# Optimization experiments

Hardware: AMD Instinct MI355X
Metric: run time of the kernel (lower is better)

The kernel has to match this reference:

```python
import jax, jax.numpy as jnp
import numpy as np

N_WIN = 7      # region grid (BiFormer default)
NUM_HEADS = 8
TOPK = 4
EPS = 1e-5

def layernorm(x, g, b):
    mu = x.mean(-1, keepdims=True)
    var = ((x - mu) ** 2).mean(-1, keepdims=True)
    return (x - mu) * jax.lax.rsqrt(var + EPS) * g + b

def bilevel_routing_attn(x, wqkv, bqkv, wo, bo):
    B, H, W, C = x.shape
    h, w = H // N_WIN, W // N_WIN          # region size (8,8)
    R, r = N_WIN * N_WIN, h * w            # 49 regions, 64 tokens each
    d = C // NUM_HEADS
    scale = 1.0 / jnp.sqrt(jnp.asarray(d, x.dtype))
    qkv = x @ wqkv + bqkv                  # (B,H,W,3C)
    q, k, v = jnp.split(qkv, 3, axis=-1)
    def to_regions(t):
        t = t.reshape(B, N_WIN, h, N_WIN, w, C).transpose(0, 1, 3, 2, 4, 5)
        return t.reshape(B, R, r, C)
    qr, kr, vr = to_regions(q), to_regions(k), to_regions(v)
    # coarse region-level routing
    q_reg = qr.mean(2)                     # (B,R,C)
    k_reg = kr.mean(2)
    logits = jnp.einsum('brc,bsc->brs', q_reg, k_reg)   # (B,R,R)
    _, idx = jax.lax.top_k(logits, TOPK)   # (B,R,TOPK)
    # gather top-k regions' k/v: out[b,i,j] = kr[b, idx[b,i,j]]
    idx_e = idx[:, :, :, None, None]       # (B,R,TOPK,1,1)
    kg = jnp.take_along_axis(kr[:, None], idx_e, axis=2).reshape(B, R, TOPK * r, C)
    vg = jnp.take_along_axis(vr[:, None], idx_e, axis=2).reshape(B, R, TOPK * r, C)
    # fine-grained multi-head attention within routed regions
    qh = qr.reshape(B, R, r, NUM_HEADS, d)
    kh = kg.reshape(B, R, TOPK * r, NUM_HEADS, d)
    vh = vg.reshape(B, R, TOPK * r, NUM_HEADS, d)
    scores = jnp.einsum('brqhd,brkhd->brhqk', qh, kh) * scale
    attn = jax.nn.softmax(scores, axis=-1)
    out = jnp.einsum('brhqk,brkhd->brqhd', attn, vh).reshape(B, R, r, C)
    # regions back to image layout
    out = out.reshape(B, N_WIN, N_WIN, h, w, C).transpose(0, 1, 3, 2, 4, 5)
    out = out.reshape(B, H, W, C)
    return out @ wo + bo

def mlp(x, w1, bm1, w2, bm2):
    return jax.nn.gelu(x @ w1 + bm1) @ w2 + bm2

def setup_inputs() -> dict:
    key = jax.random.key(0)
    ks = jax.random.split(key, 5)
    C = 256
    s = lambda fan: 1.0 / np.sqrt(fan)
    return {
        'x': jax.random.normal(ks[0], (8, 56, 56, C), jnp.float32),
        'ln1_g': jnp.ones((C,), jnp.float32),
        'ln1_b': jnp.zeros((C,), jnp.float32),
        'wqkv': jax.random.normal(ks[1], (C, 3 * C), jnp.float32) * s(C),
        'bqkv': jnp.zeros((3 * C,), jnp.float32),
        'wo': jax.random.normal(ks[2], (C, C), jnp.float32) * s(C),
        'bo': jnp.zeros((C,), jnp.float32),
        'ln2_g': jnp.ones((C,), jnp.float32),
        'ln2_b': jnp.zeros((C,), jnp.float32),
        'w1': jax.random.normal(ks[3], (C, 4 * C), jnp.float32) * s(C),
        'bm1': jnp.zeros((4 * C,), jnp.float32),
        'w2': jax.random.normal(ks[4], (4 * C, C), jnp.float32) * s(4 * C),
        'bm2': jnp.zeros((C,), jnp.float32),
    }

def reference(x, ln1_g, ln1_b, wqkv, bqkv, wo, bo, ln2_g, ln2_b, w1, bm1, w2, bm2):
    x = x + bilevel_routing_attn(layernorm(x, ln1_g, ln1_b), wqkv, bqkv, wo, bo)
    x = x + mlp(layernorm(x, ln2_g, ln2_b), w1, bm1, w2, bm2)
    return x
```

## Files before the change

### kernel.cpp

```cpp
#include <hip/hip_runtime.h>
#include <math.h>

#define CDIM 256
#define QKVDIM 768
#define NHEADS 8
#define DHEAD 32
#define NWIN 7
#define NREG 49
#define TK 4
static constexpr int NROWS = 8 * 56 * 56;

typedef __attribute__((ext_vector_type(8))) short s16x8;
typedef __attribute__((ext_vector_type(4))) float f32x4;
typedef __attribute__((ext_vector_type(16))) float f32x16;
typedef unsigned short ushort_t;

union U4 { unsigned u[4]; s16x8 v; };

__device__ __forceinline__ ushort_t bfr(float f) {
    unsigned u = __float_as_uint(f);
    unsigned r = (u + 0x7FFFu + ((u >> 16) & 1u)) >> 16;
    return (ushort_t)r;
}
__device__ __forceinline__ float gelu_f(float x) {
    float u = 0.7978845608028654f * (x + 0.044715f * x * x * x);
    return 0.5f * x * (1.0f + tanhf(u));
}
__device__ __forceinline__ void glds16(const void* g, void* l) {
    __builtin_amdgcn_global_load_lds((const __attribute__((address_space(1))) void*)g,
                                     (__attribute__((address_space(3))) void*)l, 16, 0, 0);
}
template <int N>
__device__ __forceinline__ void waitvm() {
    if constexpr (N == 0) asm volatile("s_waitcnt vmcnt(0)" ::: "memory");
    else if constexpr (N == 3) asm volatile("s_waitcnt vmcnt(3)" ::: "memory");
    else if constexpr (N == 4) asm volatile("s_waitcnt vmcnt(4)" ::: "memory");
}
__device__ __forceinline__ void barrier_raw() {
    asm volatile("s_barrier" ::: "memory");
}
__device__ __forceinline__ f32x16 zero16() {
    f32x16 z;
#pragma unroll
    for (int i = 0; i < 16; i++) z[i] = 0.f;
    return z;
}

__global__ __launch_bounds__(256) void ln_kernel(const float* __restrict__ x,
                                                 const float* __restrict__ g,
                                                 const float* __restrict__ bparam,
                                                 ushort_t* __restrict__ y) {
    int wave = threadIdx.x >> 6, lane = threadIdx.x & 63;
    int row = blockIdx.x * 4 + wave;
    const float4* xr = (const float4*)(x + (size_t)row * CDIM);
    float4 v = xr[lane];
    float s = v.x + v.y + v.z + v.w;
    float s2 = v.x * v.x + v.y * v.y + v.z * v.z + v.w * v.w;
#pragma unroll
    for (int off = 32; off; off >>= 1) {
        s += __shfl_xor(s, off, 64);
        s2 += __shfl_xor(s2, off, 64);
    }
    float mu = s * (1.0f / CDIM);
    float rstd = rsqrtf(s2 * (1.0f / CDIM) - mu * mu + 1e-5f);
    float4 gv = ((const float4*)g)[lane];
    float4 bv = ((const float4*)bparam)[lane];
    ushort4 o;
    o.x = bfr((v.x - mu) * rstd * gv.x + bv.x);
    o.y = bfr((v.y - mu) * rstd * gv.y + bv.y);
    o.z = bfr((v.z - mu) * rstd * gv.z + bv.z);
    o.w = bfr((v.w - mu) * rstd * gv.w + bv.w);
    *(ushort4*)(y + (size_t)row * CDIM + lane * 4) = o;
}

__global__ __launch_bounds__(256) void ymean_kernel(const float* __restrict__ x,
                                                    const float* __restrict__ g,
                                                    const float* __restrict__ bparam,
                                                    float* __restrict__ ymean) {
    int blk = blockIdx.x;
    int b = blk / NREG, rid = blk % NREG;
    int ai = rid / NWIN, aj = rid % NWIN;
    int w = threadIdx.x >> 6, lane = threadIdx.x & 63;
    float4 gv = ((const float4*)g)[lane];
    float4 bv = ((const float4*)bparam)[lane];
    float4 acc = {0.f, 0.f, 0.f, 0.f};
    for (int it = 0; it < 16; it++) {
        int t = it * 4 + w;
        size_t row = ((size_t)(b * 56 + ai * 8 + (t >> 3))) * 56 + aj * 8 + (t & 7);
        float4 v = ((const float4*)(x + row * CDIM))[lane];
        float s = v.x + v.y + v.z + v.w;
        float s2 = v.x * v.x + v.y * v.y + v.z * v.z + v.w * v.w;
#pragma unroll
        for (int off = 32; off; off >>= 1) {
            s += __shfl_xor(s, off, 64);
            s2 += __shfl_xor(s2, off, 64);
        }
        float mu = s * (1.0f / CDIM);
        float rstd = rsqrtf(s2 * (1.0f / CDIM) - mu * mu + 1e-5f);
        acc.x += (v.x - mu) * rstd * gv.x + bv.x;
        acc.y += (v.y - mu) * rstd * gv.y + bv.y;
        acc.z += (v.z - mu) * rstd * gv.z + bv.z;
        acc.w += (v.w - mu) * rstd * gv.w + bv.w;
    }
    __shared__ float red[4][CDIM];
    *(float4*)&red[w][lane * 4] = acc;
    __syncthreads();
    if (w == 0) {
        float4 r0 = *(float4*)&red[0][lane * 4];
        float4 r1 = *(float4*)&red[1][lane * 4];
        float4 r2 = *(float4*)&red[2][lane * 4];
        float4 r3 = *(float4*)&red[3][lane * 4];
        float4 o;
        o.x = (r0.x + r1.x + r2.x + r3.x) * (1.0f / 64.0f);
        o.y = (r0.y + r1.y + r2.y + r3.y) * (1.0f / 64.0f);
        o.z = (r0.z + r1.z + r2.z + r3.z) * (1.0f / 64.0f);
        o.w = (r0.w + r1.w + r2.w + r3.w) * (1.0f / 64.0f);
        *(float4*)(ymean + (size_t)blk * CDIM + lane * 4) = o;
    }
}

__global__ __launch_bounds__(256) void regproj_kernel(const float* __restrict__ ymean,
                                                      const float* __restrict__ wqkv,
                                                      const float* __restrict__ bqkv,
                                                      float* __restrict__ qreg,
                                                      float* __restrict__ kreg) {
    int blk = blockIdx.x;
    __shared__ float ym[CDIM];
    ym[threadIdx.x] = ymean[(size_t)blk * CDIM + threadIdx.x];
    __syncthreads();
    int c = threadIdx.x;
    float sq = 0.f, sk = 0.f;
    for (int k = 0; k < CDIM; k++) {
        float yv = ym[k];
        sq = fmaf(yv, wqkv[(size_t)k * QKVDIM + c], sq);
        sk = fmaf(yv, wqkv[(size_t)k * QKVDIM + CDIM + c], sk);
    }
    qreg[(size_t)blk * CDIM + c] = sq + bqkv[c];
    kreg[(size_t)blk * CDIM + c] = sk + bqkv[CDIM + c];
}

__global__ __launch_bounds__(256) void wtrans_kernel(const float* __restrict__ src,
                                                     ushort_t* __restrict__ dst,
                                                     int K, int N) {
    __shared__ float t[32][33];
    int tx = threadIdx.x & 31, ty = threadIdx.x >> 5;
    int n0 = blockIdx.x * 32, k0 = blockIdx.y * 32;
#pragma unroll
    for (int i = 0; i < 4; i++) t[ty + i * 8][tx] = src[(size_t)(k0 + ty + i * 8) * N + n0 + tx];
    __syncthreads();
#pragma unroll
    for (int i = 0; i < 4; i++)
        dst[(size_t)(n0 + ty + i * 8) * K + k0 + tx] = bfr(t[tx][ty + i * 8]);
}

__global__ __launch_bounds__(256) void vtrans_kernel(const ushort_t* __restrict__ qkvbf,
                                                     ushort_t* __restrict__ vt) {
    __shared__ ushort_t t[32][34];
    int tx = threadIdx.x & 31, ty = threadIdx.x >> 5;
    int t0 = blockIdx.x * 32, c0 = blockIdx.y * 32, b = blockIdx.z;
#pragma unroll
    for (int i = 0; i < 4; i++)
        t[ty + i * 8][tx] = qkvbf[((size_t)b * 3136 + t0 + ty + i * 8) * QKVDIM + 512 + c0 + tx];
    __syncthreads();
#pragma unroll
    for (int i = 0; i < 4; i++)
        vt[((size_t)b * CDIM + c0 + ty + i * 8) * 3136 + t0 + tx] = t[tx][ty + i * 8];
}

template <int BM, int BN, int MODE>
__global__ __launch_bounds__(256) void mgemm(const ushort_t* __restrict__ A,
                                             const ushort_t* __restrict__ WT,
                                             const float* __restrict__ bias,
                                             const float* __restrict__ res,
                                             float* __restrict__ outf,
                                             ushort_t* __restrict__ outb,
                                             int N, int K) {
    constexpr int WM = BM / 2, WN = BN / 2, MI = WM / 16, NI = WN / 16;
    constexpr int RA = BM / 64, RB = BN / 64, L = RA + RB;
    __shared__ __align__(16) ushort_t As[2 * BM * 32];
    __shared__ __align__(16) ushort_t Bs[2 * BN * 32];
    const int tid = threadIdx.x, lane = tid & 63, w = tid >> 6;
    const int wm = w >> 1, wn = w & 1;

    const int gx = gridDim.x;
    const int nwg = gx * gridDim.y;
    const int bid = blockIdx.y * gx + blockIdx.x;
    const int lbid = (bid & 7) * (nwg >> 3) + (bid >> 3);
    const int tm = (lbid / gx) * BM, tn = (lbid % gx) * BN;

    f32x4 acc[MI][NI];
#pragma unroll
    for (int i = 0; i < MI; i++)
#pragma unroll
        for (int j = 0; j < NI; j++) acc[i][j] = (f32x4){0.f, 0.f, 0.f, 0.f};

    auto stage = [&](int buf, int k0) {
#pragma unroll
        for (int p = 0; p < RA; p++) {
            int row = (p * 4 + w) * 16 + (lane >> 2);
            int slot = lane & 3;
            int mr = (row ^ (row >> 2)) & 3;
            glds16(A + (size_t)(tm + row) * K + k0 + ((slot ^ mr) * 8),
                   (char*)As + buf * BM * 64 + (p * 4 + w) * 1024);
        }
#pragma unroll
        for (int p = 0; p < RB; p++) {
            int row = (p * 4 + w) * 16 + (lane >> 2);
            int slot = lane & 3;
            int mr = (row ^ (row >> 2)) & 3;
            glds16(WT + (size_t)(tn + row) * K + k0 + ((slot ^ mr) * 8),
                   (char*)Bs + buf * BN * 64 + (p * 4 + w) * 1024);
        }
    };

    const int NT = K >> 5;
    const int fr = lane & 15, sl = lane >> 4;
    stage(0, 0);
    for (int kt = 0; kt < NT; ++kt) {
        int cur = kt & 1;
        if (kt + 1 < NT) {
            stage(cur ^ 1, (kt + 1) * 32);
            waitvm<L>();
        } else {
            waitvm<0>();
        }
        barrier_raw();
        s16x8 af[MI], bfv[NI];
#pragma unroll
        for (int i = 0; i < MI; i++) {
            int rowa = wm * WM + i * 16 + fr;
            int ma = (rowa ^ (rowa >> 2)) & 3;
            af[i] = *(const s16x8*)&As[cur * BM * 32 + rowa * 32 + ((sl ^ ma) * 8)];
        }
#pragma unroll
        for (int j = 0; j < NI; j++) {
            int rowb = wn * WN + j * 16 + fr;
            int mb = (rowb ^ (rowb >> 2)) & 3;
            bfv[j] = *(const s16x8*)&Bs[cur * BN * 32 + rowb * 32 + ((sl ^ mb) * 8)];
        }
#pragma unroll
        for (int i = 0; i < MI; i++)
#pragma unroll
            for (int j = 0; j < NI; j++)
                acc[i][j] = __builtin_amdgcn_mfma_f32_16x16x32_bf16(af[i], bfv[j], acc[i][j], 0, 0, 0);
        barrier_raw();
    }

    const int cl = lane & 15, gq = lane >> 4;
#pragma unroll
    for (int j = 0; j < NI; j++) {
        int col = tn + wn * WN + j * 16 + cl;
        float bb = bias[col];
#pragma unroll
        for (int i = 0; i < MI; i++) {
            int rowb = tm + wm * WM + i * 16 + gq * 4;
#pragma unroll
            for (int r = 0; r < 4; r++) {
                float v = acc[i][j][r] + bb;
                size_t off = (size_t)(rowb + r) * N + col;
                if (MODE == 0) {
                    outb[off] = bfr(col < 256 ? v * 0.17677669529663687f : v);
                } else if (MODE == 1 || MODE == 3) {
                    outf[off] = v + res[off];
                } else {
                    outb[off] = bfr(gelu_f(v));
                }
            }
        }
    }
}

__global__ __launch_bounds__(64) void routing_kernel(const float* __restrict__ qreg,
                                                     const float* __restrict__ kreg,
                                                     int* __restrict__ idx) {
    int b = blockIdx.x / NREG;
    int row = blockIdx.x % NREG;
    int lane = threadIdx.x;
    float myv = -INFINITY;
    if (lane < NREG) {
        const float* qv = qreg + ((size_t)b * NREG + row) * CDIM;
        const float* kv = kreg + ((size_t)b * NREG + lane) * CDIM;
        float s = 0.f;
        for (int c = 0; c < CDIM; c++) s += qv[c] * kv[c];
        myv = s;
    }
    for (int t = 0; t < TK; t++) {
        float v = myv;
        int ix = lane;
#pragma unroll
        for (int off = 32; off; off >>= 1) {
            float ov = __shfl_xor(v, off, 64);
            int oi = __shfl_xor(ix, off, 64);
            if (ov > v || (ov == v && oi < ix)) { v = ov; ix = oi; }
        }
        if (lane == 0) idx[((size_t)b * NREG + row) * TK + t] = ix;
        if (lane == ix) myv = -INFINITY;
    }
}

__global__ __launch_bounds__(256) void attn2_kernel(const ushort_t* __restrict__ qk,
                                                    const ushort_t* __restrict__ vt,
                                                    const int* __restrict__ idx,
                                                    ushort_t* __restrict__ outb) {
    int wid = blockIdx.x * 4 + (threadIdx.x >> 6);
    int lane = threadIdx.x & 63;
    int g = lane >> 5, col = lane & 31;
    int qh = wid & 1;
    int h = (wid >> 1) & 7;
    int rr = wid >> 4;
    int rid = rr % NREG, b = rr / NREG;
    int ai = rid / NWIN, aj = rid % NWIN;

    int qtok = qh * 32 + col;
    size_t qrow_g = ((size_t)(b * 56 + ai * 8 + (qtok >> 3))) * 56 + aj * 8 + (qtok & 7);
    const s16x8 bq0 = *(const s16x8*)(qk + qrow_g * QKVDIM + h * 32 + g * 8);
    const s16x8 bq1 = *(const s16x8*)(qk + qrow_g * QKVDIM + h * 32 + 16 + g * 8);

    const int* ip = idx + (size_t)rr * TK;
    int regs[4] = {ip[0], ip[1], ip[2], ip[3]};

    float m_run = -1e30f, l_run = 0.f;
    f32x16 o = zero16();
    const size_t vtrowbase = ((size_t)(b * CDIM + h * 32 + col)) * 3136;

#pragma unroll
    for (int rc = 0; rc < 4; rc++) {
        int reg = regs[rc];
        int rai = reg / NWIN, raj = reg % NWIN;
        s16x8 ka[2][2];
#pragma unroll
        for (int mf = 0; mf < 2; mf++) {
            int ktok = mf * 32 + col;
            size_t krow_g = ((size_t)(b * 56 + rai * 8 + (ktok >> 3))) * 56 + raj * 8 + (ktok & 7);
#pragma unroll
            for (int kd = 0; kd < 2; kd++)
                ka[mf][kd] = *(const s16x8*)(qk + krow_g * QKVDIM + 256 + h * 32 + kd * 16 + g * 8);
        }
        f32x16 s0 = zero16(), s1 = zero16();
        s0 = __builtin_amdgcn_mfma_f32_32x32x16_bf16(ka[0][0], bq0, s0, 0, 0, 0);
        s0 = __builtin_amdgcn_mfma_f32_32x32x16_bf16(ka[0][1], bq1, s0, 0, 0, 0);
        s1 = __builtin_amdgcn_mfma_f32_32x32x16_bf16(ka[1][0], bq0, s1, 0, 0, 0);
        s1 = __builtin_amdgcn_mfma_f32_32x32x16_bf16(ka[1][1], bq1, s1, 0, 0, 0);

        float tmax = -1e30f;
#pragma unroll
        for (int i = 0; i < 16; i++) tmax = fmaxf(tmax, fmaxf(s0[i], s1[i]));
        tmax = fmaxf(tmax, __shfl_xor(tmax, 32, 64));

        float m_new = fmaxf(m_run, tmax);
        float f = __expf(m_run - m_new);
        l_run *= f;
#pragma unroll
        for (int r = 0; r < 16; r++) {
            int orow = (r & 3) + 8 * (r >> 2) + 4 * g;
            float fr = __shfl(f, orow, 64);
            o[r] *= fr;
        }
        m_run = m_new;

        float tsum = 0.f;
#pragma unroll
        for (int i = 0; i < 16; i++) {
            s0[i] = __expf(s0[i] - m_run);
            s1[i] = __expf(s1[i] - m_run);
            tsum += s0[i] + s1[i];
        }
        l_run += tsum + __shfl_xor(tsum, 32, 64);

#define PVSTEP(SS, CC, KS)                                                              \
    {                                                                                   \
        unsigned wa = (unsigned)bfr(SS[CC * 8 + 0]) | ((unsigned)bfr(SS[CC * 8 + 1]) << 16); \
        unsigned wb_ = (unsigned)bfr(SS[CC * 8 + 2]) | ((unsigned)bfr(SS[CC * 8 + 3]) << 16); \
        unsigned wc = (unsigned)bfr(SS[CC * 8 + 4]) | ((unsigned)bfr(SS[CC * 8 + 5]) << 16); \
        unsigned wd = (unsigned)bfr(SS[CC * 8 + 6]) | ((unsigned)bfr(SS[CC * 8 + 7]) << 16); \
        unsigned sxa = (unsigned)__shfl_xor((int)wa, 32, 64);                           \
        unsigned sxb = (unsigned)__shfl_xor((int)wb_, 32, 64);                          \
        unsigned sxc = (unsigned)__shfl_xor((int)wc, 32, 64);                           \
        unsigned sxd = (unsigned)__shfl_xor((int)wd, 32, 64);                           \
        U4 pw;                                                                          \
        pw.u[0] = g ? sxc : wa;                                                         \
        pw.u[1] = g ? sxd : wb_;                                                        \
        pw.u[2] = g ? wc : sxa;                                                         \
        pw.u[3] = g ? wd : sxb;                                                         \
        const s16x8 vb = *(const s16x8*)(vt + vtrowbase + (size_t)(rai * 8 + KS * 2 + g) * 56 + raj * 8); \
        o = __builtin_amdgcn_mfma_f32_32x32x16_bf16(pw.v, vb, o, 0, 0, 0);              \
    }
        PVSTEP(s0, 0, 0)
        PVSTEP(s0, 1, 1)
        PVSTEP(s1, 0, 2)
        PVSTEP(s1, 1, 3)
#undef PVSTEP
    }

#pragma unroll
    for (int r = 0; r < 16; r++) {
        int orow = (r & 3) + 8 * (r >> 2) + 4 * g;
        float lr = __shfl(l_run, orow, 64);
        float val = o[r] / lr;
        int tok = qh * 32 + orow;
        size_t row_g = ((size_t)(b * 56 + ai * 8 + (tok >> 3))) * 56 + aj * 8 + (tok & 7);
        outb[row_g * 256 + h * 32 + col] = bfr(val);
    }
}

extern "C" void kernel_launch(void* const* d_in, const int* in_sizes, int n_in,
                              void* d_out, int out_size, void* d_ws, size_t ws_size,
                              hipStream_t stream) {
    const float* x    = (const float*)d_in[0];
    const float* ln1g = (const float*)d_in[1];
    const float* ln1b = (const float*)d_in[2];
    const float* wqkv = (const float*)d_in[3];
    const float* bqkv = (const float*)d_in[4];
    const float* wo   = (const float*)d_in[5];
    const float* bo   = (const float*)d_in[6];
    const float* ln2g = (const float*)d_in[7];
    const float* ln2b = (const float*)d_in[8];
    const float* w1   = (const float*)d_in[9];
    const float* bm1  = (const float*)d_in[10];
    const float* w2   = (const float*)d_in[11];
    const float* bm2  = (const float*)d_in[12];
    float* out = (float*)d_out;
    char* ws = (char*)d_ws;

    ushort_t* ws_qkvbf = (ushort_t*)(ws);
    ushort_t* ws_hbf   = (ushort_t*)(ws + 38535168);
    ushort_t* ws_ybf   = (ushort_t*)(ws + 89915392);
    ushort_t* ws_vt    = (ushort_t*)(ws + 102760448);
    ushort_t* ws_attn  = (ushort_t*)(ws + 115605504);
    float*    ws_ymean = (float*)(ws + 128450560);
    float*    ws_qreg  = (float*)(ws + 128851968);
    float*    ws_kreg  = (float*)(ws + 129253376);
    int*      ws_idx   = (int*)(ws + 129654784);
    ushort_t* ws_wqkvT = (ushort_t*)(ws + 129661056);
    ushort_t* ws_woT   = (ushort_t*)(ws + 130054272);
    ushort_t* ws_w1T   = (ushort_t*)(ws + 130185344);
    ushort_t* ws_w2T   = (ushort_t*)(ws + 130709632);

    const int M = NROWS;

    wtrans_kernel<<<dim3(768 / 32, 256 / 32), 256, 0, stream>>>(wqkv, ws_wqkvT, 256, 768);
    wtrans_kernel<<<dim3(256 / 32, 256 / 32), 256, 0, stream>>>(wo, ws_woT, 256, 256);
    wtrans_kernel<<<dim3(1024 / 32, 256 / 32), 256, 0, stream>>>(w1, ws_w1T, 256, 1024);
    wtrans_kernel<<<dim3(256 / 32, 1024 / 32), 256, 0, stream>>>(w2, ws_w2T, 1024, 256);
    ln_kernel<<<M / 4, 256, 0, stream>>>(x, ln1g, ln1b, ws_ybf);
    ymean_kernel<<<8 * NREG, 256, 0, stream>>>(x, ln1g, ln1b, ws_ymean);
    regproj_kernel<<<8 * NREG, 256, 0, stream>>>(ws_ymean, wqkv, bqkv, ws_qreg, ws_kreg);
    routing_kernel<<<8 * NREG, 64, 0, stream>>>(ws_qreg, ws_kreg, ws_idx);
    mgemm<128, 128, 0><<<dim3(QKVDIM / 128, M / 128), 256, 0, stream>>>(
        ws_ybf, ws_wqkvT, bqkv, nullptr, nullptr, ws_qkvbf, QKVDIM, CDIM);
    vtrans_kernel<<<dim3(3136 / 32, 256 / 32, 8), 256, 0, stream>>>(ws_qkvbf, ws_vt);
    attn2_kernel<<<8 * NREG * NHEADS * 2 / 4, 256, 0, stream>>>(ws_qkvbf, ws_vt, ws_idx, ws_attn);
    mgemm<128, 64, 1><<<dim3(CDIM / 64, M / 128), 256, 0, stream>>>(
        ws_attn, ws_woT, bo, x, out, nullptr, CDIM, CDIM);
    ln_kernel<<<M / 4, 256, 0, stream>>>(out, ln2g, ln2b, ws_ybf);
    mgemm<128, 128, 2><<<dim3(1024 / 128, M / 128), 256, 0, stream>>>(
        ws_ybf, ws_w1T, bm1, nullptr, nullptr, ws_hbf, 1024, CDIM);
    mgemm<128, 64, 3><<<dim3(CDIM / 64, M / 128), 256, 0, stream>>>(
        ws_hbf, ws_w2T, bm2, out, out, nullptr, CDIM, 1024);
}
```

Before: 321.4 us.

## Stage bf16 GEMM epilogue through shared memory for vectorized stores, cheaper GELU

For the QKV and MLP-up GEMM modes, the epilogue now writes bf16 results into a padded shared-memory tile, reusing the A/B staging buffer. It then emits 16-byte row-contiguous global stores, replacing scattered 2-byte writes. The swizzle pattern for the LDS tiles changes to (row>>1)&3, and GELU's tanhf is replaced by an exp-based fast formula. The epilogue adds two block barriers and LDS traffic, and the fast exp GELU may differ slightly numerically.

```diff
diff --git a/kernel.cpp b/kernel.cpp
--- a/kernel.cpp
+++ b/kernel.cpp
@@ -24,7 +24,9 @@
 }
 __device__ __forceinline__ float gelu_f(float x) {
     float u = 0.7978845608028654f * (x + 0.044715f * x * x * x);
-    return 0.5f * x * (1.0f + tanhf(u));
+    float e = __expf(2.0f * u);
+    float t = 1.0f - __fdividef(2.0f, e + 1.0f);
+    return 0.5f * x * (1.0f + t);
 }
 __device__ __forceinline__ void glds16(const void* g, void* l) {
     __builtin_amdgcn_global_load_lds((const __attribute__((address_space(1))) void*)g,
@@ -177,8 +179,10 @@
                                              int N, int K) {
     constexpr int WM = BM / 2, WN = BN / 2, MI = WM / 16, NI = WN / 16;
     constexpr int RA = BM / 64, RB = BN / 64, L = RA + RB;
-    __shared__ __align__(16) ushort_t As[2 * BM * 32];
-    __shared__ __align__(16) ushort_t Bs[2 * BN * 32];
+    __shared__ __align__(16) char smem[2 * (BM + BN) * 64];
+    ushort_t* As = (ushort_t*)smem;
+    ushort_t* Bs = (ushort_t*)(smem + 2 * BM * 64);
+    ushort_t* Cs = (ushort_t*)smem;
     const int tid = threadIdx.x, lane = tid & 63, w = tid >> 6;
     const int wm = w >> 1, wn = w & 1;
 
@@ -199,7 +203,7 @@
         for (int p = 0; p < RA; p++) {
             int row = (p * 4 + w) * 16 + (lane >> 2);
             int slot = lane & 3;
-            int mr = (row ^ (row >> 2)) & 3;
+            int mr = (row >> 1) & 3;
             glds16(A + (size_t)(tm + row) * K + k0 + ((slot ^ mr) * 8),
                    (char*)As + buf * BM * 64 + (p * 4 + w) * 1024);
         }
@@ -207,7 +211,7 @@
         for (int p = 0; p < RB; p++) {
             int row = (p * 4 + w) * 16 + (lane >> 2);
             int slot = lane & 3;
-            int mr = (row ^ (row >> 2)) & 3;
+            int mr = (row >> 1) & 3;
             glds16(WT + (size_t)(tn + row) * K + k0 + ((slot ^ mr) * 8),
                    (char*)Bs + buf * BN * 64 + (p * 4 + w) * 1024);
         }
@@ -229,13 +233,13 @@
 #pragma unroll
         for (int i = 0; i < MI; i++) {
             int rowa = wm * WM + i * 16 + fr;
-            int ma = (rowa ^ (rowa >> 2)) & 3;
+            int ma = (rowa >> 1) & 3;
             af[i] = *(const s16x8*)&As[cur * BM * 32 + rowa * 32 + ((sl ^ ma) * 8)];
         }
 #pragma unroll
         for (int j = 0; j < NI; j++) {
             int rowb = wn * WN + j * 16 + fr;
-            int mb = (rowb ^ (rowb >> 2)) & 3;
+            int mb = (rowb >> 1) & 3;
             bfv[j] = *(const s16x8*)&Bs[cur * BN * 32 + rowb * 32 + ((sl ^ mb) * 8)];
         }
 #pragma unroll
@@ -247,23 +251,56 @@
     }
 
     const int cl = lane & 15, gq = lane >> 4;
-#pragma unroll
-    for (int j = 0; j < NI; j++) {
-        int col = tn + wn * WN + j * 16 + cl;
-        float bb = bias[col];
-#pragma unroll
-        for (int i = 0; i < MI; i++) {
-            int rowb = tm + wm * WM + i * 16 + gq * 4;
-#pragma unroll
-            for (int r = 0; r < 4; r++) {
-                float v = acc[i][j][r] + bb;
-                size_t off = (size_t)(rowb + r) * N + col;
-                if (MODE == 0) {
-                    outb[off] = bfr(col < 256 ? v * 0.17677669529663687f : v);
-                } else if (MODE == 1 || MODE == 3) {
+    if constexpr (MODE == 0 || MODE == 2) {
+#pragma unroll
+        for (int hh = 0; hh < 2; hh++) {
+            if (wm == hh) {
+#pragma unroll
+                for (int j = 0; j < NI; j++) {
+                    int lcol = wn * WN + j * 16 + cl;
+                    int col = tn + lcol;
+                    float bb = bias[col];
+#pragma unroll
+                    for (int i = 0; i < MI; i++) {
+#pragma unroll
+                        for (int r = 0; r < 4; r++) {
+                            float v = acc[i][j][r] + bb;
+                            ushort_t ov;
+                            if (MODE == 0)
+                                ov = bfr(col < 256 ? v * 0.17677669529663687f : v);
+                            else
+                                ov = bfr(gelu_f(v));
+                            Cs[(i * 16 + gq * 4 + r) * 136 + lcol] = ov;
+                        }
+                    }
+                }
+            }
+            __syncthreads();
+            {
+                int row_l = tid >> 2;
+                int cb = (tid & 3) * 8;
+                ushort_t* gbase = outb + (size_t)(tm + hh * 64 + row_l) * N + tn;
+#pragma unroll
+                for (int c = 0; c < 4; c++) {
+                    int col = cb + c * 32;
+                    *(s16x8*)(gbase + col) = *(const s16x8*)&Cs[row_l * 136 + col];
+                }
+            }
+            if (hh == 0) __syncthreads();
+        }
+    } else {
+#pragma unroll
+        for (int j = 0; j < NI; j++) {
+            int col = tn + wn * WN + j * 16 + cl;
+            float bb = bias[col];
+#pragma unroll
+            for (int i = 0; i < MI; i++) {
+                int rowb = tm + wm * WM + i * 16 + gq * 4;
+#pragma unroll
+                for (int r = 0; r < 4; r++) {
+                    float v = acc[i][j][r] + bb;
+                    size_t off = (size_t)(rowb + r) * N + col;
                     outf[off] = v + res[off];
-                } else {
-                    outb[off] = bfr(gelu_f(v));
                 }
             }
         }
```

After: 314.4 us. 1.02x faster.
